# Kernel optimization log

Hardware: AMD Instinct MI355X
Metric: run time of the kernel (lower is better)

The kernel has to match this reference:

```python
import jax, jax.numpy as jnp
import numpy as np


def _pairwise_mse_gram(x):
    """G[i, j] = mean_d (x[i, d] - x[j, d])**2, computed in closed form.

    Replaces the original O(N^2) Python double loop over F.mse_loss with a
    single GEMM: |x_i|^2 + |x_j|^2 - 2 x_i . x_j, divided by D.
    """
    x = x.reshape(x.shape[0], -1)            # [N, D]
    D = x.shape[1]
    sq = jnp.sum(x * x, axis=1)              # [N]
    gram = x @ x.T                           # [N, N] GEMM
    return (sq[:, None] + sq[None, :] - 2.0 * gram) / D


def setup_inputs() -> dict:
    key = jax.random.key(0)
    k1, k2 = jax.random.split(key)
    fm_s = jax.random.normal(k1, (1024, 64, 16, 16), dtype=jnp.float32)
    fm_t = jax.random.normal(k2, (1024, 64, 16, 16), dtype=jnp.float32)
    return {"fm_s": fm_s, "fm_t": fm_t}


def reference(fm_s, fm_t):
    # Faithful to the original source, including its bug: the second double
    # loop writes the teacher pairwise-MSE matrix into G_s (overwriting the
    # student one entirely), while G_t stays all-zeros. Hence the final loss
    # is mse(pairwise_mse_gram(fm_t), 0) and fm_s does not affect the output.
    G_s = _pairwise_mse_gram(fm_t)           # [N, N]
    G_t = jnp.zeros_like(G_s)
    return jnp.mean((G_s - G_t) ** 2)
```

## Files before the change

kernel.cpp:

```cpp
#include <hip/hip_runtime.h>
#include <hip/hip_bf16.h>
#include <stdint.h>

#define N_ROWS 1024
#define KDIM   16384

typedef __attribute__((ext_vector_type(8))) __bf16 bf16x8;
typedef __attribute__((ext_vector_type(4))) float  f32x4;

#define GLOBAL_AS __attribute__((address_space(1)))
#define LDS_AS    __attribute__((address_space(3)))

__device__ __forceinline__ unsigned short f32_to_bf16_rne(float f) {
    unsigned int u = __float_as_uint(f);
    unsigned int lsb = (u >> 16) & 1u;
    u += 0x7fffu + lsb;
    return (unsigned short)(u >> 16);
}

__global__ __launch_bounds__(256) void cast_sq_kernel(
        const float* __restrict__ X, unsigned short* __restrict__ Xb,
        float* __restrict__ sq) {
    const int row = blockIdx.x;
    const float4* src = (const float4*)(X + (size_t)row * KDIM);
    uint2* dst = (uint2*)(Xb + (size_t)row * KDIM);
    float ss = 0.f;
#pragma unroll
    for (int c = 0; c < 16; ++c) {
        int idx = c * 256 + threadIdx.x;
        float4 v = src[idx];
        ss += v.x * v.x + v.y * v.y + v.z * v.z + v.w * v.w;
        uint2 p;
        p.x = (unsigned int)f32_to_bf16_rne(v.x) | ((unsigned int)f32_to_bf16_rne(v.y) << 16);
        p.y = (unsigned int)f32_to_bf16_rne(v.z) | ((unsigned int)f32_to_bf16_rne(v.w) << 16);
        dst[idx] = p;
    }
#pragma unroll
    for (int o = 32; o; o >>= 1) ss += __shfl_down(ss, o, 64);
    __shared__ float red[4];
    int lane = threadIdx.x & 63, wv = threadIdx.x >> 6;
    if (lane == 0) red[wv] = ss;
    __syncthreads();
    if (threadIdx.x == 0) sq[row] = red[0] + red[1] + red[2] + red[3];
}

__global__ __launch_bounds__(256) void gram_gemm_kernel(
        const unsigned short* __restrict__ Xb, float* __restrict__ G) {
    __shared__ unsigned short As[128 * 64];
    __shared__ unsigned short Bs[128 * 64];

    const int row0 = blockIdx.x * 128;
    const int col0 = blockIdx.y * 128;
    const int kbeg = blockIdx.z * (KDIM / 8);
    const int kend = kbeg + (KDIM / 8);

    const int tid  = threadIdx.x;
    const int lane = tid & 63;
    const int wv   = tid >> 6;
    const int wm   = (wv >> 1) * 64;
    const int wn   = (wv & 1) * 64;
    const int lr   = lane & 15;
    const int lk   = (lane >> 4) * 8;

    f32x4 acc[4][4] = {};

    for (int k0 = kbeg; k0 < kend; k0 += 64) {
#pragma unroll
        for (int it = 0; it < 4; ++it) {
            int c  = it * 256 + tid;
            int r  = c >> 3;
            int kc = (c & 7) << 3;
            const unsigned short* ga = Xb + (size_t)(row0 + r) * KDIM + k0 + kc;
            const unsigned short* gb = Xb + (size_t)(col0 + r) * KDIM + k0 + kc;
            __builtin_amdgcn_global_load_lds((GLOBAL_AS void*)(void*)ga,
                                             (LDS_AS void*)&As[c * 8], 16, 0, 0);
            __builtin_amdgcn_global_load_lds((GLOBAL_AS void*)(void*)gb,
                                             (LDS_AS void*)&Bs[c * 8], 16, 0, 0);
        }
        __syncthreads();

#pragma unroll
        for (int s = 0; s < 2; ++s) {
            const int ko = s * 32 + lk;
            bf16x8 af[4], bfq[4];
#pragma unroll
            for (int i = 0; i < 4; ++i)
                af[i] = *(const bf16x8*)&As[(wm + i * 16 + lr) * 64 + ko];
#pragma unroll
            for (int j = 0; j < 4; ++j)
                bfq[j] = *(const bf16x8*)&Bs[(wn + j * 16 + lr) * 64 + ko];
#pragma unroll
            for (int i = 0; i < 4; ++i)
#pragma unroll
                for (int j = 0; j < 4; ++j)
                    acc[i][j] = __builtin_amdgcn_mfma_f32_16x16x32_bf16(
                        af[i], bfq[j], acc[i][j], 0, 0, 0);
        }
        __syncthreads();
    }

    const int crow0 = row0 + wm + (lane >> 4) * 4;
    const int ccol0 = col0 + wn + (lane & 15);
#pragma unroll
    for (int i = 0; i < 4; ++i)
#pragma unroll
        for (int j = 0; j < 4; ++j)
#pragma unroll
            for (int r = 0; r < 4; ++r) {
                int grow = crow0 + i * 16 + r;
                int gcol = ccol0 + j * 16;
                atomicAdd(&G[(size_t)grow * N_ROWS + gcol], acc[i][j][r]);
            }
}

__global__ __launch_bounds__(256) void loss_kernel(
        const float* __restrict__ G, const float* __restrict__ sq,
        float* __restrict__ out) {
    const float invD = 1.0f / (float)KDIM;
    float acc = 0.f;
    for (int idx = blockIdx.x * 256 + threadIdx.x; idx < N_ROWS * N_ROWS;
         idx += gridDim.x * 256) {
        int i = idx >> 10;
        int j = idx & (N_ROWS - 1);
        float v = (sq[i] + sq[j] - 2.0f * G[idx]) * invD;
        acc += v * v;
    }
#pragma unroll
    for (int o = 32; o; o >>= 1) acc += __shfl_down(acc, o, 64);
    __shared__ float red[4];
    int lane = threadIdx.x & 63, wv = threadIdx.x >> 6;
    if (lane == 0) red[wv] = acc;
    __syncthreads();
    if (threadIdx.x == 0) {
        float total = red[0] + red[1] + red[2] + red[3];
        atomicAdd(out, total * (1.0f / ((float)N_ROWS * (float)N_ROWS)));
    }
}

extern "C" void kernel_launch(void* const* d_in, const int* in_sizes, int n_in,
                              void* d_out, int out_size, void* d_ws, size_t ws_size,
                              hipStream_t stream) {
    const float* fm_t = (const float*)d_in[1];
    float* out = (float*)d_out;

    char* ws = (char*)d_ws;
    unsigned short* Xb = (unsigned short*)ws;
    float* sq = (float*)(ws + (size_t)N_ROWS * KDIM * 2);
    float* G  = (float*)(ws + (size_t)N_ROWS * KDIM * 2 + 4096);

    hipMemsetAsync(G, 0, (size_t)N_ROWS * N_ROWS * sizeof(float), stream);
    hipMemsetAsync(out, 0, sizeof(float), stream);

    cast_sq_kernel<<<dim3(N_ROWS), 256, 0, stream>>>(fm_t, Xb, sq);
    gram_gemm_kernel<<<dim3(8, 8, 8), 256, 0, stream>>>(Xb, G);
    loss_kernel<<<dim3(256), 256, 0, stream>>>(G, sq, out);
}
```

Before: 205.9 us.

## Exploit Gram symmetry with triangular tiles, swizzle LDS, raise split-K

The GEMM now computes only the 36 upper-triangular 128x128 tiles of the symmetric Gram matrix, using a constant lookup table, and split-K goes from 8 to 16 so the grid stays large. The loss kernel reads only those tiles and weights off-diagonal tiles by two. LDS layout gains an XOR swizzle on the 16-byte chunks to cut bank conflicts on the fragment reads. This roughly halves the MFMA work and the atomic traffic, at the cost of more split-K atomics per tile and table lookups in the loss loop.

```diff
diff --git a/kernel.cpp b/kernel.cpp
--- a/kernel.cpp
+++ b/kernel.cpp
@@ -4,12 +4,19 @@
 
 #define N_ROWS 1024
 #define KDIM   16384
+#define SPLITK 16
+#define KBLK   (KDIM / SPLITK)
 
 typedef __attribute__((ext_vector_type(8))) __bf16 bf16x8;
 typedef __attribute__((ext_vector_type(4))) float  f32x4;
 
 #define GLOBAL_AS __attribute__((address_space(1)))
 #define LDS_AS    __attribute__((address_space(3)))
+
+__device__ __constant__ unsigned char T_I[36] = {
+    0,0,0,0,0,0,0,0, 1,1,1,1,1,1,1, 2,2,2,2,2,2, 3,3,3,3,3, 4,4,4,4, 5,5,5, 6,6, 7};
+__device__ __constant__ unsigned char T_J[36] = {
+    0,1,2,3,4,5,6,7, 1,2,3,4,5,6,7, 2,3,4,5,6,7, 3,4,5,6,7, 4,5,6,7, 5,6,7, 6,7, 7};
 
 __device__ __forceinline__ unsigned short f32_to_bf16_rne(float f) {
     unsigned int u = __float_as_uint(f);
@@ -49,10 +56,12 @@
     __shared__ unsigned short As[128 * 64];
     __shared__ unsigned short Bs[128 * 64];
 
-    const int row0 = blockIdx.x * 128;
-    const int col0 = blockIdx.y * 128;
-    const int kbeg = blockIdx.z * (KDIM / 8);
-    const int kend = kbeg + (KDIM / 8);
+    const int ti = T_I[blockIdx.x];
+    const int tj = T_J[blockIdx.x];
+    const int row0 = ti * 128;
+    const int col0 = tj * 128;
+    const int kbeg = blockIdx.y * KBLK;
+    const int kend = kbeg + KBLK;
 
     const int tid  = threadIdx.x;
     const int lane = tid & 63;
@@ -60,7 +69,8 @@
     const int wm   = (wv >> 1) * 64;
     const int wn   = (wv & 1) * 64;
     const int lr   = lane & 15;
-    const int lk   = (lane >> 4) * 8;
+    const int lq   = lane >> 4;
+    const int swz  = lr & 7;
 
     f32x4 acc[4][4] = {};
 
@@ -69,9 +79,10 @@
         for (int it = 0; it < 4; ++it) {
             int c  = it * 256 + tid;
             int r  = c >> 3;
-            int kc = (c & 7) << 3;
-            const unsigned short* ga = Xb + (size_t)(row0 + r) * KDIM + k0 + kc;
-            const unsigned short* gb = Xb + (size_t)(col0 + r) * KDIM + k0 + kc;
+            int j  = c & 7;
+            int js = j ^ (r & 7);
+            const unsigned short* ga = Xb + (size_t)(row0 + r) * KDIM + k0 + js * 8;
+            const unsigned short* gb = Xb + (size_t)(col0 + r) * KDIM + k0 + js * 8;
             __builtin_amdgcn_global_load_lds((GLOBAL_AS void*)(void*)ga,
                                              (LDS_AS void*)&As[c * 8], 16, 0, 0);
             __builtin_amdgcn_global_load_lds((GLOBAL_AS void*)(void*)gb,
@@ -81,14 +92,15 @@
 
 #pragma unroll
         for (int s = 0; s < 2; ++s) {
-            const int ko = s * 32 + lk;
+            const int kch = s * 4 + lq;
+            const int slot = (kch ^ swz) * 8;
             bf16x8 af[4], bfq[4];
 #pragma unroll
             for (int i = 0; i < 4; ++i)
-                af[i] = *(const bf16x8*)&As[(wm + i * 16 + lr) * 64 + ko];
+                af[i] = *(const bf16x8*)&As[(wm + i * 16 + lr) * 64 + slot];
 #pragma unroll
             for (int j = 0; j < 4; ++j)
-                bfq[j] = *(const bf16x8*)&Bs[(wn + j * 16 + lr) * 64 + ko];
+                bfq[j] = *(const bf16x8*)&Bs[(wn + j * 16 + lr) * 64 + slot];
 #pragma unroll
             for (int i = 0; i < 4; ++i)
 #pragma unroll
@@ -99,8 +111,8 @@
         __syncthreads();
     }
 
-    const int crow0 = row0 + wm + (lane >> 4) * 4;
-    const int ccol0 = col0 + wn + (lane & 15);
+    const int crow0 = row0 + wm + lq * 4;
+    const int ccol0 = col0 + wn + lr;
 #pragma unroll
     for (int i = 0; i < 4; ++i)
 #pragma unroll
@@ -117,13 +129,17 @@
         const float* __restrict__ G, const float* __restrict__ sq,
         float* __restrict__ out) {
     const float invD = 1.0f / (float)KDIM;
+    const int TOT = 36 * 128 * 128;
     float acc = 0.f;
-    for (int idx = blockIdx.x * 256 + threadIdx.x; idx < N_ROWS * N_ROWS;
-         idx += gridDim.x * 256) {
-        int i = idx >> 10;
-        int j = idx & (N_ROWS - 1);
-        float v = (sq[i] + sq[j] - 2.0f * G[idx]) * invD;
-        acc += v * v;
+    for (int u = blockIdx.x * 256 + threadIdx.x; u < TOT; u += gridDim.x * 256) {
+        int t = u >> 14;
+        int e = u & 16383;
+        int i = T_I[t] * 128 + (e >> 7);
+        int j = T_J[t] * 128 + (e & 127);
+        float g = G[i * N_ROWS + j];
+        float v = (sq[i] + sq[j] - 2.0f * g) * invD;
+        float w = (T_I[t] == T_J[t]) ? 1.0f : 2.0f;
+        acc += w * v * v;
     }
 #pragma unroll
     for (int o = 32; o; o >>= 1) acc += __shfl_down(acc, o, 64);
@@ -145,13 +161,13 @@
 
     char* ws = (char*)d_ws;
     unsigned short* Xb = (unsigned short*)ws;
-    float* sq = (float*)(ws + (size_t)N_ROWS * KDIM * 2);
-    float* G  = (float*)(ws + (size_t)N_ROWS * KDIM * 2 + 4096);
+    float* G  = (float*)(ws + (size_t)N_ROWS * KDIM * 2);
+    float* sq = (float*)(ws + (size_t)N_ROWS * KDIM * 2 + (size_t)N_ROWS * N_ROWS * 4);
 
     hipMemsetAsync(G, 0, (size_t)N_ROWS * N_ROWS * sizeof(float), stream);
     hipMemsetAsync(out, 0, sizeof(float), stream);
 
     cast_sq_kernel<<<dim3(N_ROWS), 256, 0, stream>>>(fm_t, Xb, sq);
-    gram_gemm_kernel<<<dim3(8, 8, 8), 256, 0, stream>>>(Xb, G);
+    gram_gemm_kernel<<<dim3(36, SPLITK), 256, 0, stream>>>(Xb, G);
     loss_kernel<<<dim3(256), 256, 0, stream>>>(G, sq, out);
 }
```

Measured after the change: 206.3 us. Within noise of the previous version (+0.2%).
